# Kernel tuning notes

Hardware: AMD Instinct MI355X
Metric: run time of the kernel (lower is better)

Reference implementation:

```python
import jax, jax.numpy as jnp
import numpy as np

# config
B, V, S, D = 2, 8, 256, 2048
NH, NKV, KVR = 32, 8, 2
HD = D // NH            # 64
G = NH // NKV           # GQA group size = 4
INIT = 0.02


def _neighbor_idx():
    # replicates generate_neighbor: left neighbors (i-half..i-1) then right (i+1..i+half), circular
    half = KVR // 2
    offsets = np.concatenate([np.arange(-half, 0), np.arange(1, half + 1)])
    return (np.arange(V)[:, None] + offsets[None, :]) % V  # [V, KVR]


def setup_inputs() -> dict:
    key = jax.random.key(0)
    k1, k2, k3, k4 = jax.random.split(key, 4)
    x = jax.random.normal(k1, (B, V, S, D), jnp.float32)
    wq = jax.random.normal(k2, (D, NH * HD), jnp.float32) * INIT
    wkv = jax.random.normal(k3, (D, 2 * NKV * HD), jnp.float32) * INIT
    wo = jax.random.normal(k4, (D, D), jnp.float32) * INIT
    return {"x": x, "wq": wq, "wkv": wkv, "wo": wo}


def reference(x, wq, wkv, wo):
    b, v, s, d = x.shape
    idx = _neighbor_idx()  # [V, KVR] static

    # Q projection: [b, v, s, NH*HD]
    xq = (x @ wq).reshape(b, v, s, NKV, G, HD)  # grouped-query layout (kv head, group)

    # neighbor gather: [b, v, KVR, s, d] -> [b, v, KVR*s, d]
    x_kv = x[:, idx].reshape(b, v, KVR * s, d)
    kv = x_kv @ wkv
    xk, xv = jnp.split(kv, 2, axis=-1)
    xk = xk.reshape(b, v, KVR * s, NKV, HD)
    xv = xv.reshape(b, v, KVR * s, NKV, HD)

    # grouped-query SDPA (no mask, eval mode): avoids materializing repeated K/V
    scale = 1.0 / jnp.sqrt(jnp.asarray(HD, x.dtype))
    scores = jnp.einsum('bvsngh,bvtnh->bvngst', xq, xk) * scale  # [b,v,NKV,G,s,KVR*s]
    attn = jax.nn.softmax(scores, axis=-1)
    out = jnp.einsum('bvngst,bvtnh->bvsngh', attn, xv).reshape(b, v, s, d)
    return out @ wo
```

## Files before the change

### kernel.cpp

```cpp
#include <hip/hip_runtime.h>
#include <stdint.h>

typedef unsigned short u16;
typedef unsigned int   u32;
typedef short short8 __attribute__((ext_vector_type(8)));
typedef float f32x4  __attribute__((ext_vector_type(4)));

__device__ __forceinline__ u16 f2bf(float f){
  u32 u = __builtin_bit_cast(u32, f);
  u32 r = (u + 0x7FFFu + ((u >> 16) & 1u)) >> 16;
  return (u16)r;
}
__device__ __forceinline__ u32 cvtpk(float a, float b){
  u32 r; asm("v_cvt_pk_bf16_f32 %0, %1, %2" : "=v"(r) : "v"(a), "v"(b)); return r;
}
__device__ __forceinline__ void gload16(const u16* g, u16* l){
  __builtin_amdgcn_global_load_lds((const __attribute__((address_space(1))) void*)g,
                                   (__attribute__((address_space(3))) void*)l, 16, 0, 0);
}
#define BARRIER()  do{ __builtin_amdgcn_s_barrier(); __builtin_amdgcn_sched_barrier(0); }while(0)

__global__ __launch_bounds__(256) void k_cvt_bf16(const float* __restrict__ x,
                                                  u16* __restrict__ y, int n8){
  int i = blockIdx.x * 256 + threadIdx.x;
  if (i >= n8) return;
  const float4* p = (const float4*)x + (size_t)i * 2;
  float4 a = p[0], b = p[1];
  short8 o;
  o[0] = f2bf(a.x); o[1] = f2bf(a.y); o[2] = f2bf(a.z); o[3] = f2bf(a.w);
  o[4] = f2bf(b.x); o[5] = f2bf(b.y); o[6] = f2bf(b.z); o[7] = f2bf(b.w);
  *(short8*)(y + (size_t)i * 8) = o;
}

__global__ __launch_bounds__(256) void k_transpose_w(const float* __restrict__ in,
                                                     u16* __restrict__ out, int R, int C){
  __shared__ float tile[32][33];
  int nc = C >> 5;
  int cb = blockIdx.x % nc, rb = blockIdx.x / nc;
  int tx = threadIdx.x & 31, ty = threadIdx.x >> 5;
#pragma unroll
  for (int i = 0; i < 4; ++i){
    int r = rb * 32 + ty + i * 8;
    tile[ty + i * 8][tx] = in[(size_t)r * C + cb * 32 + tx];
  }
  __syncthreads();
#pragma unroll
  for (int i = 0; i < 4; ++i){
    int c = cb * 32 + ty + i * 8;
    out[(size_t)c * R + rb * 32 + tx] = f2bf(tile[tx][ty + i * 8]);
  }
}

template<int BM, int BN, int MH, int NFRAG, int ALOADS, int BLOADS, bool QSCALE, typename CT>
__global__ __launch_bounds__(512, 1) void k_gemm8p(const u16* __restrict__ A,
                                                   const u16* __restrict__ Bt,
                                                   CT* __restrict__ C,
                                                   int N, int K){
  constexpr int SZA = BM * 128;
  constexpr int SZB = BN * 128;
  constexpr int SZ  = SZA + SZB;
  constexpr int WTM = BM / 2;
  constexpr int WTN = BN / 4;
  __shared__ char lds[2 * SZ];

  int tid = threadIdx.x, lane = tid & 63, wid = tid >> 6;
  int l16 = lane & 15, g4 = lane >> 4;
  int wm = wid >> 2, wn = wid & 3;
  int bid = blockIdx.x;
  int wg = (bid & 7) * 32 + (bid >> 3);
  int nb = N / BN;
  int bm = wg / nb, bn = wg % nb;

  const u16* baseA = A  + (size_t)(bm * BM) * K;
  const u16* baseB = Bt + (size_t)(bn * BN) * K;

  int aLds[ALOADS], aG[ALOADS];
#pragma unroll
  for (int i = 0; i < ALOADS; ++i){
    int q = (wid * ALOADS + i) * 1024 + lane * 16;
    int row = q >> 7, c = q & 127;
    int cs = c ^ ((row & 7) << 4);
    aLds[i] = q; aG[i] = row * K + (cs >> 1);
  }
  int bLds[BLOADS], bG[BLOADS];
#pragma unroll
  for (int j = 0; j < BLOADS; ++j){
    int q = (wid * BLOADS + j) * 1024 + lane * 16;
    int row = q >> 7, c = q & 127;
    int cs = c ^ ((row & 7) << 4);
    bLds[j] = q; bG[j] = row * K + (cs >> 1);
  }
  auto stageA = [&](int t){
    char* dst = lds + (t & 1) * SZ;
#pragma unroll
    for (int i = 0; i < ALOADS; ++i) gload16(baseA + aG[i] + t * 64, (u16*)(dst + aLds[i]));
  };
  auto stageB = [&](int t){
    char* dst = lds + (t & 1) * SZ + SZA;
#pragma unroll
    for (int j = 0; j < BLOADS; ++j) gload16(baseB + bG[j] + t * 64, (u16*)(dst + bLds[j]));
  };
  auto rdA = [&](const char* Ab, int m, int ks){
    int row = wm * WTM + m * 16 + l16;
    return *(const short8*)(Ab + row * 128 + ((ks * 64 + g4 * 16) ^ ((row & 7) << 4)));
  };
  auto rdB = [&](const char* Bb, int nf, int ks){
    int row = wn * WTN + nf * 16 + l16;
    return *(const short8*)(Bb + row * 128 + ((ks * 64 + g4 * 16) ^ ((row & 7) << 4)));
  };

  f32x4 zero4 = {0.f, 0.f, 0.f, 0.f};
  f32x4 acc[2 * MH][NFRAG];
#pragma unroll
  for (int i = 0; i < 2 * MH; ++i)
#pragma unroll
    for (int j = 0; j < NFRAG; ++j) acc[i][j] = zero4;

  int NK = K >> 6;
  stageA(0); stageB(0);
  asm volatile("s_waitcnt vmcnt(0)" ::: "memory");
  BARRIER();
  short8 a0[MH], a1[MH], a2[MH], a3[MH], bf0[NFRAG], bf1[NFRAG];
#pragma unroll
  for (int nf = 0; nf < NFRAG; ++nf) bf0[nf] = rdB(lds + SZA, nf, 0);
#pragma unroll
  for (int m = 0; m < MH; ++m)       a0[m]  = rdA(lds, m, 0);

  for (int kt = 0; kt < NK; ++kt){
    const char* Ab = lds + (kt & 1) * SZ;
    const char* Bb = Ab + SZA;
    bool st = (kt + 1 < NK);
#pragma unroll
    for (int m = 0; m < MH; ++m) a1[m] = rdA(Ab, MH + m, 0);
    if (st) stageA(kt + 1);
    BARRIER();
    __builtin_amdgcn_s_setprio(1);
#pragma unroll
    for (int m = 0; m < MH; ++m)
#pragma unroll
      for (int nf = 0; nf < NFRAG; ++nf)
        acc[m][nf] = __builtin_amdgcn_mfma_f32_16x16x32_bf16(a0[m], bf0[nf], acc[m][nf], 0, 0, 0);
    __builtin_amdgcn_s_setprio(0);
#pragma unroll
    for (int nf = 0; nf < NFRAG; ++nf) bf1[nf] = rdB(Bb, nf, 1);
#pragma unroll
    for (int m = 0; m < MH; ++m)       a2[m]  = rdA(Ab, m, 1);
    if (st) stageB(kt + 1);
    BARRIER();
    __builtin_amdgcn_s_setprio(1);
#pragma unroll
    for (int m = 0; m < MH; ++m)
#pragma unroll
      for (int nf = 0; nf < NFRAG; ++nf)
        acc[MH + m][nf] = __builtin_amdgcn_mfma_f32_16x16x32_bf16(a1[m], bf0[nf], acc[MH + m][nf], 0, 0, 0);
    __builtin_amdgcn_s_setprio(0);
#pragma unroll
    for (int m = 0; m < MH; ++m) a3[m] = rdA(Ab, MH + m, 1);
    BARRIER();
    __builtin_amdgcn_s_setprio(1);
#pragma unroll
    for (int m = 0; m < MH; ++m)
#pragma unroll
      for (int nf = 0; nf < NFRAG; ++nf)
        acc[m][nf] = __builtin_amdgcn_mfma_f32_16x16x32_bf16(a2[m], bf1[nf], acc[m][nf], 0, 0, 0);
    __builtin_amdgcn_s_setprio(0);
    if (st) asm volatile("s_waitcnt vmcnt(0)" ::: "memory");
    BARRIER();
    if (st){
      const char* Ab2 = lds + ((kt + 1) & 1) * SZ;
      const char* Bb2 = Ab2 + SZA;
#pragma unroll
      for (int nf = 0; nf < NFRAG; ++nf) bf0[nf] = rdB(Bb2, nf, 0);
#pragma unroll
      for (int m = 0; m < MH; ++m)       a0[m]  = rdA(Ab2, m, 0);
    }
    __builtin_amdgcn_s_setprio(1);
#pragma unroll
    for (int m = 0; m < MH; ++m)
#pragma unroll
      for (int nf = 0; nf < NFRAG; ++nf)
        acc[MH + m][nf] = __builtin_amdgcn_mfma_f32_16x16x32_bf16(a3[m], bf1[nf], acc[MH + m][nf], 0, 0, 0);
    __builtin_amdgcn_s_setprio(0);
    BARRIER();
  }

#pragma unroll
  for (int mf = 0; mf < 2 * MH; ++mf)
#pragma unroll
    for (int nf = 0; nf < NFRAG; ++nf)
#pragma unroll
      for (int r = 0; r < 4; ++r){
        int row = bm * BM + wm * WTM + mf * 16 + g4 * 4 + r;
        int col = bn * BN + wn * WTN + nf * 16 + l16;
        float vv = acc[mf][nf][r];
        if constexpr (QSCALE) { if (col < 2048) vv *= 0.18033688011112042f; }
        if constexpr (sizeof(CT) == 2) C[(size_t)row * N + col] = (CT)f2bf(vv);
        else                           C[(size_t)row * N + col] = (CT)vv;
      }
}

__global__ __launch_bounds__(256) void k_vt(const u16* __restrict__ c1, u16* __restrict__ vt){
  __shared__ u16 tile[64][72];
  int bid = blockIdx.x;
  int st = bid & 3, n = (bid >> 2) & 7, bv = bid >> 5;
  int t = threadIdx.x;
  int sr = t >> 2, sc = t & 3;
  const u16* src = c1 + (size_t)(bv * 256 + st * 64 + sr) * 3072 + 2560 + n * 64 + sc * 16;
  short8 a = *(const short8*)src;
  short8 b = *(const short8*)(src + 8);
  *(short8*)&tile[sr][sc * 16]     = a;
  *(short8*)&tile[sr][sc * 16 + 8] = b;
  __syncthreads();
  int h = t >> 2, c2 = t & 3;
  short8 o0, o1;
#pragma unroll
  for (int j = 0; j < 8; ++j) o0[j] = (short)tile[c2 * 16 + j][h];
#pragma unroll
  for (int j = 0; j < 8; ++j) o1[j] = (short)tile[c2 * 16 + 8 + j][h];
  u16* dst = vt + (size_t)((bv * 8 + n) * 64 + h) * 256 + st * 64 + c2 * 16;
  *(short8*)dst       = o0;
  *(short8*)(dst + 8) = o1;
}

__global__ __launch_bounds__(256, 2) void k_attn(const u16* __restrict__ c1,
                                                 const u16* __restrict__ vt,
                                                 u16* __restrict__ att){
  __shared__ u16 Klds[64][72];
  __shared__ u16 Vlds[64][72];
  __shared__ u16 Plds[4][16][72];
  int bid = blockIdx.x;
  int qt = bid & 3, n = (bid >> 2) & 7, v = (bid >> 5) & 7, b = bid >> 8;
  int tid = threadIdx.x;
  int g = tid >> 6, lane = tid & 63, l16 = lane & 15, g4 = lane >> 4;
  int bv = b * 8 + v;
  int rowQ = bv * 256 + qt * 64;
  int qcol = n * 256 + g * 64;

  short8 qf[4][2];
#pragma unroll
  for (int qi = 0; qi < 4; ++qi)
#pragma unroll
    for (int kk = 0; kk < 2; ++kk)
      qf[qi][kk] = *(const short8*)(c1 + (size_t)(rowQ + qi * 16 + l16) * 3072
                                     + qcol + kk * 32 + g4 * 8);

  f32x4 zero4 = {0.f, 0.f, 0.f, 0.f};
  f32x4 O[4][4];
#pragma unroll
  for (int i = 0; i < 4; ++i)
#pragma unroll
    for (int j = 0; j < 4; ++j) O[i][j] = zero4;
  float m2[4]   = {-3.0e38f, -3.0e38f, -3.0e38f, -3.0e38f};
  float lsum[4] = {0.f, 0.f, 0.f, 0.f};

  int sr = tid >> 2, sc = tid & 3;
  short8 k0, k1, v0, v1;
  {
    int vn = (v + 7) & 7;
    const u16* ks = c1 + (size_t)((b * 8 + vn) * 256 + sr) * 3072 + 2048 + n * 64 + sc * 16;
    k0 = *(const short8*)ks; k1 = *(const short8*)(ks + 8);
    const u16* vs = vt + (size_t)(((b * 8 + vn) * 8 + n) * 64 + sr) * 256 + sc * 16;
    v0 = *(const short8*)vs; v1 = *(const short8*)(vs + 8);
  }

  for (int ti = 0; ti < 8; ++ti){
    __syncthreads();
    *(short8*)&Klds[sr][sc * 16]     = k0;
    *(short8*)&Klds[sr][sc * 16 + 8] = k1;
    *(short8*)&Vlds[sr][sc * 16]     = v0;
    *(short8*)&Vlds[sr][sc * 16 + 8] = v1;
    __syncthreads();
    if (ti < 7){
      int tn = ti + 1;
      int vn = (tn < 4) ? ((v + 7) & 7) : ((v + 1) & 7);
      int tb = (tn & 3) * 64;
      const u16* ks = c1 + (size_t)((b * 8 + vn) * 256 + tb + sr) * 3072 + 2048 + n * 64 + sc * 16;
      k0 = *(const short8*)ks; k1 = *(const short8*)(ks + 8);
      const u16* vs = vt + (size_t)(((b * 8 + vn) * 8 + n) * 64 + sr) * 256 + tb + sc * 16;
      v0 = *(const short8*)vs; v1 = *(const short8*)(vs + 8);
    }
    short8 kf[4][2], vf[2][4];
#pragma unroll
    for (int kt = 0; kt < 4; ++kt)
#pragma unroll
      for (int ks = 0; ks < 2; ++ks)
        kf[kt][ks] = *(const short8*)&Klds[kt * 16 + l16][ks * 32 + g4 * 8];
#pragma unroll
    for (int ks = 0; ks < 2; ++ks)
#pragma unroll
      for (int hi = 0; hi < 4; ++hi)
        vf[ks][hi] = *(const short8*)&Vlds[hi * 16 + l16][ks * 32 + g4 * 8];

#pragma unroll
    for (int qi = 0; qi < 4; ++qi){
      f32x4 sa[4];
#pragma unroll
      for (int kt = 0; kt < 4; ++kt){
        sa[kt] = zero4;
#pragma unroll
        for (int ks = 0; ks < 2; ++ks)
          sa[kt] = __builtin_amdgcn_mfma_f32_16x16x32_bf16(kf[kt][ks], qf[qi][ks], sa[kt], 0, 0, 0);
      }
      float pmax = sa[0][0];
#pragma unroll
      for (int kt = 0; kt < 4; ++kt)
#pragma unroll
        for (int r = 0; r < 4; ++r) pmax = fmaxf(pmax, sa[kt][r]);
      pmax = fmaxf(pmax, __shfl_xor(pmax, 16));
      pmax = fmaxf(pmax, __shfl_xor(pmax, 32));
      if (__any(pmax > m2[qi] + 8.f)){
        float mnew  = fmaxf(m2[qi], pmax);
        float alpha = exp2f(m2[qi] - mnew);
        m2[qi] = mnew;
        lsum[qi] *= alpha;
        float ab[4];
#pragma unroll
        for (int r = 0; r < 4; ++r) ab[r] = __shfl(alpha, g4 * 4 + r);
#pragma unroll
        for (int hi = 0; hi < 4; ++hi)
#pragma unroll
          for (int r = 0; r < 4; ++r) O[qi][hi][r] *= ab[r];
      }
      float m = m2[qi];
      float psum = 0.f;
      u32 w[4][2];
#pragma unroll
      for (int kt = 0; kt < 4; ++kt){
        float p0 = exp2f(sa[kt][0] - m);
        float p1 = exp2f(sa[kt][1] - m);
        float p2 = exp2f(sa[kt][2] - m);
        float p3 = exp2f(sa[kt][3] - m);
        psum += (p0 + p1) + (p2 + p3);
        w[kt][0] = cvtpk(p0, p1);
        w[kt][1] = cvtpk(p2, p3);
      }
      psum += __shfl_xor(psum, 16);
      psum += __shfl_xor(psum, 32);
      lsum[qi] += psum;
      u32* prow = (u32*)&Plds[g][l16][0];
#pragma unroll
      for (int kt = 0; kt < 4; ++kt){
        prow[kt * 8 + g4 * 2]     = w[kt][0];
        prow[kt * 8 + g4 * 2 + 1] = w[kt][1];
      }
      short8 pa[2];
#pragma unroll
      for (int ks = 0; ks < 2; ++ks)
        pa[ks] = *(const short8*)&Plds[g][l16][ks * 32 + g4 * 8];
#pragma unroll
      for (int hi = 0; hi < 4; ++hi)
#pragma unroll
        for (int ks = 0; ks < 2; ++ks)
          O[qi][hi] = __builtin_amdgcn_mfma_f32_16x16x32_bf16(pa[ks], vf[ks][hi], O[qi][hi], 0, 0, 0);
    }
  }
#pragma unroll
  for (int qi = 0; qi < 4; ++qi){
    float lb[4];
#pragma unroll
    for (int r = 0; r < 4; ++r) lb[r] = 1.0f / __shfl(lsum[qi], g4 * 4 + r);
#pragma unroll
    for (int hi = 0; hi < 4; ++hi)
#pragma unroll
      for (int r = 0; r < 4; ++r){
        int row = rowQ + qi * 16 + g4 * 4 + r;
        int col = qcol + hi * 16 + l16;
        att[(size_t)row * 2048 + col] = f2bf(O[qi][hi][r] * lb[r]);
      }
  }
}

extern "C" void kernel_launch(void* const* d_in, const int* in_sizes, int n_in,
                              void* d_out, int out_size, void* d_ws, size_t ws_size,
                              hipStream_t stream){
  const float* x   = (const float*)d_in[0];
  const float* wq  = (const float*)d_in[1];
  const float* wkv = (const float*)d_in[2];
  const float* wo  = (const float*)d_in[3];
  float* out = (float*)d_out;
  char* ws = (char*)d_ws;

  u16* x_bf  = (u16*)(ws);
  u16* wqkvt = (u16*)(ws + 16777216);
  u16* wot   = (u16*)(ws + 29360128);
  u16* c1    = (u16*)(ws + 37748736);
  u16* vt    = (u16*)(ws + 62914560);
  u16* att   = x_bf;

  k_cvt_bf16<<<4096, 256, 0, stream>>>(x, x_bf, 1048576);
  k_transpose_w<<<4096, 256, 0, stream>>>(wq,  wqkvt,               2048, 2048);
  k_transpose_w<<<2048, 256, 0, stream>>>(wkv, wqkvt + 2048 * 2048, 2048, 1024);
  k_transpose_w<<<4096, 256, 0, stream>>>(wo,  wot,                 2048, 2048);
  k_gemm8p<256, 192, 4, 3, 4, 3, true,  u16  ><<<256, 512, 0, stream>>>(x_bf, wqkvt, c1, 3072, 2048);
  k_vt<<<512, 256, 0, stream>>>(c1, vt);
  k_attn<<<512, 256, 0, stream>>>(c1, vt, att);
  k_gemm8p<128, 256, 2, 4, 2, 4, false, float><<<256, 512, 0, stream>>>(att, wot, out, 2048, 2048);
}
```

Before: 154.7 us.

## Pre-swizzle weights into MFMA fragment order and load B directly to registers

The weight-transpose kernels become a prep kernel that writes bf16 weights in the exact per-wave MFMA fragment layout. The GEMM then loads B fragments straight from global memory into registers, prefetched one k-tile ahead, instead of staging them through LDS. This removes B LDS traffic and its share of the LDS footprint, so more waves may fit per CU now that the launch bound no longer forces one block. The cost is more register pressure for the double-buffered B fragments, and B reuse across the two wave rows now depends on the cache instead of LDS.

```diff
diff --git a/kernel.cpp b/kernel.cpp
--- a/kernel.cpp
+++ b/kernel.cpp
@@ -32,36 +32,45 @@
   *(short8*)(y + (size_t)i * 8) = o;
 }
 
-__global__ __launch_bounds__(256) void k_transpose_w(const float* __restrict__ in,
-                                                     u16* __restrict__ out, int R, int C){
-  __shared__ float tile[32][33];
+template<int MODE>
+__global__ __launch_bounds__(256) void k_prepw(const float* __restrict__ w,
+                                               u16* __restrict__ Bp, int C, int noff){
+  __shared__ float tile[64][33];
   int nc = C >> 5;
-  int cb = blockIdx.x % nc, rb = blockIdx.x / nc;
-  int tx = threadIdx.x & 31, ty = threadIdx.x >> 5;
-#pragma unroll
-  for (int i = 0; i < 4; ++i){
-    int r = rb * 32 + ty + i * 8;
-    tile[ty + i * 8][tx] = in[(size_t)r * C + cb * 32 + tx];
-  }
+  int cb = blockIdx.x % nc;
+  int kt = blockIdx.x / nc;
+  int t = threadIdx.x;
+  int kl = t >> 5, c = t & 31;
+#pragma unroll
+  for (int i = 0; i < 8; ++i)
+    tile[kl + i * 8][c] = w[(size_t)(kt * 64 + kl + i * 8) * C + cb * 32 + c];
   __syncthreads();
-#pragma unroll
-  for (int i = 0; i < 4; ++i){
-    int c = cb * 32 + ty + i * 8;
-    out[(size_t)c * R + rb * 32 + tx] = f2bf(tile[tx][ty + i * 8]);
-  }
-}
-
-template<int BM, int BN, int MH, int NFRAG, int ALOADS, int BLOADS, bool QSCALE, typename CT>
-__global__ __launch_bounds__(512, 1) void k_gemm8p(const u16* __restrict__ A,
-                                                   const u16* __restrict__ Bt,
-                                                   CT* __restrict__ C,
-                                                   int N, int K){
+  int l16 = t & 15, g4 = (t >> 4) & 3, ks = (t >> 6) & 1, nh = t >> 7;
+  int n = noff + cb * 32 + nh * 16 + l16;
+  int kb = ks * 32 + g4 * 8;
+  short8 o;
+#pragma unroll
+  for (int e = 0; e < 8; ++e) o[e] = (short)f2bf(tile[kb + e][nh * 16 + l16]);
+  size_t dst;
+  if constexpr (MODE == 0){
+    int bn = n / 192, r = n % 192, wn = r / 48, r2 = r % 48, nf = r2 / 16, L = r2 % 16;
+    dst = ((((size_t)(bn * 4 + wn) * 32 + kt) * 2 + ks) * 3 + nf) * 512 + (g4 * 16 + L) * 8;
+  } else {
+    int bn = n >> 8, wn = (n >> 6) & 3, nf = (n >> 4) & 3, L = n & 15;
+    dst = ((((size_t)(bn * 4 + wn) * 32 + kt) * 2 + ks) * 4 + nf) * 512 + (g4 * 16 + L) * 8;
+  }
+  *(short8*)(Bp + dst) = o;
+}
+
+template<int BM, int NF, int MH, int ALOADS, bool QSCALE, typename CT>
+__global__ __launch_bounds__(512) void k_gemm_bd(const u16* __restrict__ A,
+                                                 const u16* __restrict__ Bp,
+                                                 CT* __restrict__ C,
+                                                 int N, int K){
+  constexpr int BN  = NF * 64;
+  constexpr int WTM = BM / 2;
   constexpr int SZA = BM * 128;
-  constexpr int SZB = BN * 128;
-  constexpr int SZ  = SZA + SZB;
-  constexpr int WTM = BM / 2;
-  constexpr int WTN = BN / 4;
-  __shared__ char lds[2 * SZ];
+  __shared__ char lds[2 * SZA];
 
   int tid = threadIdx.x, lane = tid & 63, wid = tid >> 6;
   int l16 = lane & 15, g4 = lane >> 4;
@@ -71,8 +80,8 @@
   int nb = N / BN;
   int bm = wg / nb, bn = wg % nb;
 
-  const u16* baseA = A  + (size_t)(bm * BM) * K;
-  const u16* baseB = Bt + (size_t)(bn * BN) * K;
+  const u16* baseA  = A  + (size_t)(bm * BM) * K;
+  const u16* baseBp = Bp + (size_t)(bn * 4 + wn) * (32 * 2 * NF * 512) + lane * 8;
 
   int aLds[ALOADS], aG[ALOADS];
 #pragma unroll
@@ -82,116 +91,106 @@
     int cs = c ^ ((row & 7) << 4);
     aLds[i] = q; aG[i] = row * K + (cs >> 1);
   }
-  int bLds[BLOADS], bG[BLOADS];
-#pragma unroll
-  for (int j = 0; j < BLOADS; ++j){
-    int q = (wid * BLOADS + j) * 1024 + lane * 16;
-    int row = q >> 7, c = q & 127;
-    int cs = c ^ ((row & 7) << 4);
-    bLds[j] = q; bG[j] = row * K + (cs >> 1);
-  }
   auto stageA = [&](int t){
-    char* dst = lds + (t & 1) * SZ;
+    char* dst = lds + (t & 1) * SZA;
 #pragma unroll
     for (int i = 0; i < ALOADS; ++i) gload16(baseA + aG[i] + t * 64, (u16*)(dst + aLds[i]));
-  };
-  auto stageB = [&](int t){
-    char* dst = lds + (t & 1) * SZ + SZA;
-#pragma unroll
-    for (int j = 0; j < BLOADS; ++j) gload16(baseB + bG[j] + t * 64, (u16*)(dst + bLds[j]));
   };
   auto rdA = [&](const char* Ab, int m, int ks){
     int row = wm * WTM + m * 16 + l16;
     return *(const short8*)(Ab + row * 128 + ((ks * 64 + g4 * 16) ^ ((row & 7) << 4)));
   };
-  auto rdB = [&](const char* Bb, int nf, int ks){
-    int row = wn * WTN + nf * 16 + l16;
-    return *(const short8*)(Bb + row * 128 + ((ks * 64 + g4 * 16) ^ ((row & 7) << 4)));
+  auto loadB = [&](short8* dst, int t){
+    const u16* p = baseBp + (size_t)t * (2 * NF * 512);
+#pragma unroll
+    for (int j = 0; j < 2 * NF; ++j) dst[j] = *(const short8*)(p + j * 512);
   };
 
   f32x4 zero4 = {0.f, 0.f, 0.f, 0.f};
-  f32x4 acc[2 * MH][NFRAG];
+  f32x4 acc[2 * MH][NF];
 #pragma unroll
   for (int i = 0; i < 2 * MH; ++i)
 #pragma unroll
-    for (int j = 0; j < NFRAG; ++j) acc[i][j] = zero4;
+    for (int j = 0; j < NF; ++j) acc[i][j] = zero4;
+
+  short8 bf[2 * NF], bfn[2 * NF];
+  short8 ac[MH], an[MH], a2[MH], a3[MH];
 
   int NK = K >> 6;
-  stageA(0); stageB(0);
+  stageA(0);
+  loadB(bf, 0);
   asm volatile("s_waitcnt vmcnt(0)" ::: "memory");
   BARRIER();
-  short8 a0[MH], a1[MH], a2[MH], a3[MH], bf0[NFRAG], bf1[NFRAG];
-#pragma unroll
-  for (int nf = 0; nf < NFRAG; ++nf) bf0[nf] = rdB(lds + SZA, nf, 0);
-#pragma unroll
-  for (int m = 0; m < MH; ++m)       a0[m]  = rdA(lds, m, 0);
+#pragma unroll
+  for (int m = 0; m < MH; ++m) ac[m] = rdA(lds, m, 0);
 
   for (int kt = 0; kt < NK; ++kt){
-    const char* Ab = lds + (kt & 1) * SZ;
-    const char* Bb = Ab + SZA;
+    const char* Ab = lds + (kt & 1) * SZA;
     bool st = (kt + 1 < NK);
 #pragma unroll
-    for (int m = 0; m < MH; ++m) a1[m] = rdA(Ab, MH + m, 0);
+    for (int m = 0; m < MH; ++m) an[m] = rdA(Ab, MH + m, 0);
     if (st) stageA(kt + 1);
     BARRIER();
     __builtin_amdgcn_s_setprio(1);
 #pragma unroll
     for (int m = 0; m < MH; ++m)
 #pragma unroll
-      for (int nf = 0; nf < NFRAG; ++nf)
-        acc[m][nf] = __builtin_amdgcn_mfma_f32_16x16x32_bf16(a0[m], bf0[nf], acc[m][nf], 0, 0, 0);
+      for (int nf = 0; nf < NF; ++nf)
+        acc[m][nf] = __builtin_amdgcn_mfma_f32_16x16x32_bf16(ac[m], bf[nf], acc[m][nf], 0, 0, 0);
     __builtin_amdgcn_s_setprio(0);
 #pragma unroll
-    for (int nf = 0; nf < NFRAG; ++nf) bf1[nf] = rdB(Bb, nf, 1);
-#pragma unroll
-    for (int m = 0; m < MH; ++m)       a2[m]  = rdA(Ab, m, 1);
-    if (st) stageB(kt + 1);
+    for (int m = 0; m < MH; ++m) a2[m] = rdA(Ab, m, 1);
     BARRIER();
     __builtin_amdgcn_s_setprio(1);
 #pragma unroll
     for (int m = 0; m < MH; ++m)
 #pragma unroll
-      for (int nf = 0; nf < NFRAG; ++nf)
-        acc[MH + m][nf] = __builtin_amdgcn_mfma_f32_16x16x32_bf16(a1[m], bf0[nf], acc[MH + m][nf], 0, 0, 0);
+      for (int nf = 0; nf < NF; ++nf)
+        acc[MH + m][nf] = __builtin_amdgcn_mfma_f32_16x16x32_bf16(an[m], bf[nf], acc[MH + m][nf], 0, 0, 0);
     __builtin_amdgcn_s_setprio(0);
 #pragma unroll
     for (int m = 0; m < MH; ++m) a3[m] = rdA(Ab, MH + m, 1);
+    if (st) loadB(bfn, kt + 1);
     BARRIER();
     __builtin_amdgcn_s_setprio(1);
 #pragma unroll
     for (int m = 0; m < MH; ++m)
 #pragma unroll
-      for (int nf = 0; nf < NFRAG; ++nf)
-        acc[m][nf] = __builtin_amdgcn_mfma_f32_16x16x32_bf16(a2[m], bf1[nf], acc[m][nf], 0, 0, 0);
+      for (int nf = 0; nf < NF; ++nf)
+        acc[m][nf] = __builtin_amdgcn_mfma_f32_16x16x32_bf16(a2[m], bf[NF + nf], acc[m][nf], 0, 0, 0);
     __builtin_amdgcn_s_setprio(0);
-    if (st) asm volatile("s_waitcnt vmcnt(0)" ::: "memory");
-    BARRIER();
     if (st){
-      const char* Ab2 = lds + ((kt + 1) & 1) * SZ;
-      const char* Bb2 = Ab2 + SZA;
-#pragma unroll
-      for (int nf = 0; nf < NFRAG; ++nf) bf0[nf] = rdB(Bb2, nf, 0);
-#pragma unroll
-      for (int m = 0; m < MH; ++m)       a0[m]  = rdA(Ab2, m, 0);
+      if constexpr (NF == 3) asm volatile("s_waitcnt vmcnt(6)" ::: "memory");
+      else                   asm volatile("s_waitcnt vmcnt(8)" ::: "memory");
+    }
+    BARRIER();
+    if (st){
+      const char* Ab2 = lds + ((kt + 1) & 1) * SZA;
+#pragma unroll
+      for (int m = 0; m < MH; ++m) ac[m] = rdA(Ab2, m, 0);
     }
     __builtin_amdgcn_s_setprio(1);
 #pragma unroll
     for (int m = 0; m < MH; ++m)
 #pragma unroll
-      for (int nf = 0; nf < NFRAG; ++nf)
-        acc[MH + m][nf] = __builtin_amdgcn_mfma_f32_16x16x32_bf16(a3[m], bf1[nf], acc[MH + m][nf], 0, 0, 0);
+      for (int nf = 0; nf < NF; ++nf)
+        acc[MH + m][nf] = __builtin_amdgcn_mfma_f32_16x16x32_bf16(a3[m], bf[NF + nf], acc[MH + m][nf], 0, 0, 0);
     __builtin_amdgcn_s_setprio(0);
+    if (st){
+#pragma unroll
+      for (int j = 0; j < 2 * NF; ++j) bf[j] = bfn[j];
+    }
     BARRIER();
   }
 
 #pragma unroll
   for (int mf = 0; mf < 2 * MH; ++mf)
 #pragma unroll
-    for (int nf = 0; nf < NFRAG; ++nf)
+    for (int nf = 0; nf < NF; ++nf)
 #pragma unroll
       for (int r = 0; r < 4; ++r){
         int row = bm * BM + wm * WTM + mf * 16 + g4 * 4 + r;
-        int col = bn * BN + wn * WTN + nf * 16 + l16;
+        int col = bn * BN + wn * (NF * 16) + nf * 16 + l16;
         float vv = acc[mf][nf][r];
         if constexpr (QSCALE) { if (col < 2048) vv *= 0.18033688011112042f; }
         if constexpr (sizeof(CT) == 2) C[(size_t)row * N + col] = (CT)f2bf(vv);
@@ -380,19 +379,19 @@
   float* out = (float*)d_out;
   char* ws = (char*)d_ws;
 
-  u16* x_bf  = (u16*)(ws);
-  u16* wqkvt = (u16*)(ws + 16777216);
-  u16* wot   = (u16*)(ws + 29360128);
-  u16* c1    = (u16*)(ws + 37748736);
-  u16* vt    = (u16*)(ws + 62914560);
-  u16* att   = x_bf;
+  u16* x_bf   = (u16*)(ws);
+  u16* bp_qkv = (u16*)(ws + 16777216);
+  u16* bp_o   = (u16*)(ws + 29360128);
+  u16* c1     = (u16*)(ws + 37748736);
+  u16* vt     = (u16*)(ws + 62914560);
+  u16* att    = x_bf;
 
   k_cvt_bf16<<<4096, 256, 0, stream>>>(x, x_bf, 1048576);
-  k_transpose_w<<<4096, 256, 0, stream>>>(wq,  wqkvt,               2048, 2048);
-  k_transpose_w<<<2048, 256, 0, stream>>>(wkv, wqkvt + 2048 * 2048, 2048, 1024);
-  k_transpose_w<<<4096, 256, 0, stream>>>(wo,  wot,                 2048, 2048);
-  k_gemm8p<256, 192, 4, 3, 4, 3, true,  u16  ><<<256, 512, 0, stream>>>(x_bf, wqkvt, c1, 3072, 2048);
+  k_prepw<0><<<2048, 256, 0, stream>>>(wq,  bp_qkv, 2048, 0);
+  k_prepw<0><<<1024, 256, 0, stream>>>(wkv, bp_qkv, 1024, 2048);
+  k_prepw<1><<<2048, 256, 0, stream>>>(wo,  bp_o,   2048, 0);
+  k_gemm_bd<256, 3, 4, 4, true,  u16  ><<<256, 512, 0, stream>>>(x_bf, bp_qkv, c1, 3072, 2048);
   k_vt<<<512, 256, 0, stream>>>(c1, vt);
   k_attn<<<512, 256, 0, stream>>>(c1, vt, att);
-  k_gemm8p<128, 256, 2, 4, 2, 4, false, float><<<256, 512, 0, stream>>>(att, wot, out, 2048, 2048);
-}
+  k_gemm_bd<128, 4, 2, 2, false, float><<<256, 512, 0, stream>>>(att, bp_o, out, 2048, 2048);
+}
```

New measurement: 180.7 us. 16.8% more time.

## Restructure GEMM main loop with finer-grained staged loads and partial vmcnt waits

Applied to the files above, without the earlier changes.

Replaces the GEMM kernel with a variant that splits next-tile global-to-LDS loads into per-slab stages spread across the four MFMA phases. It uses partial s_waitcnt vmcnt counts instead of a full drain before the buffer swap. It also changes the A-tile row-to-wave mapping and the LDS load addressing, and drops the min-blocks launch bound. The aim is to overlap global loads with MFMA work more evenly and reduce stalls at barriers. This adds extra barriers per k-step and risks correctness if the partial wait counts do not cover the slabs that are read next.

```diff
diff --git a/kernel.cpp b/kernel.cpp
--- a/kernel.cpp
+++ b/kernel.cpp
@@ -51,16 +51,16 @@
   }
 }
 
-template<int BM, int BN, int MH, int NFRAG, int ALOADS, int BLOADS, bool QSCALE, typename CT>
-__global__ __launch_bounds__(512, 1) void k_gemm8p(const u16* __restrict__ A,
-                                                   const u16* __restrict__ Bt,
-                                                   CT* __restrict__ C,
-                                                   int N, int K){
+template<int BM, int BN, int MFR, int NF, bool QSCALE, typename CT>
+__global__ __launch_bounds__(512) void k_gemm8m(const u16* __restrict__ A,
+                                                const u16* __restrict__ Bt,
+                                                CT* __restrict__ C,
+                                                int N, int K){
+  constexpr int MH  = MFR / 2;
+  constexpr int AL  = BM / 64, BL = BN / 64, L = AL + BL;
   constexpr int SZA = BM * 128;
-  constexpr int SZB = BN * 128;
-  constexpr int SZ  = SZA + SZB;
-  constexpr int WTM = BM / 2;
-  constexpr int WTN = BN / 4;
+  constexpr int SZ  = (BM + BN) * 128;
+  constexpr int F3  = (MFR == 8) ? 2 : 1;
   __shared__ char lds[2 * SZ];
 
   int tid = threadIdx.x, lane = tid & 63, wid = tid >> 6;
@@ -74,124 +74,133 @@
   const u16* baseA = A  + (size_t)(bm * BM) * K;
   const u16* baseB = Bt + (size_t)(bn * BN) * K;
 
-  int aLds[ALOADS], aG[ALOADS];
-#pragma unroll
-  for (int i = 0; i < ALOADS; ++i){
-    int q = (wid * ALOADS + i) * 1024 + lane * 16;
+  int aG[AL], bG[BL];
+#pragma unroll
+  for (int i = 0; i < AL; ++i){
+    int q = i * 8192 + tid * 16;
     int row = q >> 7, c = q & 127;
     int cs = c ^ ((row & 7) << 4);
-    aLds[i] = q; aG[i] = row * K + (cs >> 1);
-  }
-  int bLds[BLOADS], bG[BLOADS];
-#pragma unroll
-  for (int j = 0; j < BLOADS; ++j){
-    int q = (wid * BLOADS + j) * 1024 + lane * 16;
+    aG[i] = row * K + (cs >> 1);
+  }
+#pragma unroll
+  for (int j = 0; j < BL; ++j){
+    int q = j * 8192 + tid * 16;
     int row = q >> 7, c = q & 127;
     int cs = c ^ ((row & 7) << 4);
-    bLds[j] = q; bG[j] = row * K + (cs >> 1);
-  }
-  auto stageA = [&](int t){
+    bG[j] = row * K + (cs >> 1);
+  }
+  auto stageL = [&](int t, int l){
     char* dst = lds + (t & 1) * SZ;
-#pragma unroll
-    for (int i = 0; i < ALOADS; ++i) gload16(baseA + aG[i] + t * 64, (u16*)(dst + aLds[i]));
+    if (l < BL){
+      gload16(baseB + bG[l] + t * 64, (u16*)(dst + SZA + l * 8192 + tid * 16));
+    } else {
+      int i;
+      if constexpr (MFR == 8){ constexpr int ord[4] = {0, 2, 1, 3}; i = ord[l - BL]; }
+      else                   { i = l - BL; }
+      gload16(baseA + aG[i] + t * 64, (u16*)(dst + i * 8192 + tid * 16));
+    }
   };
-  auto stageB = [&](int t){
-    char* dst = lds + (t & 1) * SZ + SZA;
-#pragma unroll
-    for (int j = 0; j < BLOADS; ++j) gload16(baseB + bG[j] + t * 64, (u16*)(dst + bLds[j]));
+  auto aRowBase = [&](int mf){
+    if constexpr (MFR == 8) return wm * 128 + mf * 16;
+    else                    return (mf >> 1) * 64 + wm * 32 + (mf & 1) * 16;
   };
-  auto rdA = [&](const char* Ab, int m, int ks){
-    int row = wm * WTM + m * 16 + l16;
-    return *(const short8*)(Ab + row * 128 + ((ks * 64 + g4 * 16) ^ ((row & 7) << 4)));
+  auto rdA = [&](const char* buf, int mf, int ks){
+    int row = aRowBase(mf) + l16;
+    return *(const short8*)(buf + row * 128 + ((ks * 64 + g4 * 16) ^ ((row & 7) << 4)));
   };
-  auto rdB = [&](const char* Bb, int nf, int ks){
-    int row = wn * WTN + nf * 16 + l16;
-    return *(const short8*)(Bb + row * 128 + ((ks * 64 + g4 * 16) ^ ((row & 7) << 4)));
+  auto rdB = [&](const char* buf, int nf, int ks){
+    int row = wn * (NF * 16) + nf * 16 + l16;
+    return *(const short8*)(buf + SZA + row * 128 + ((ks * 64 + g4 * 16) ^ ((row & 7) << 4)));
   };
 
   f32x4 zero4 = {0.f, 0.f, 0.f, 0.f};
-  f32x4 acc[2 * MH][NFRAG];
-#pragma unroll
-  for (int i = 0; i < 2 * MH; ++i)
-#pragma unroll
-    for (int j = 0; j < NFRAG; ++j) acc[i][j] = zero4;
+  f32x4 acc[MFR][NF];
+#pragma unroll
+  for (int i = 0; i < MFR; ++i)
+#pragma unroll
+    for (int j = 0; j < NF; ++j) acc[i][j] = zero4;
 
   int NK = K >> 6;
-  stageA(0); stageB(0);
+#pragma unroll
+  for (int l = 0; l < L; ++l) stageL(0, l);
   asm volatile("s_waitcnt vmcnt(0)" ::: "memory");
   BARRIER();
-  short8 a0[MH], a1[MH], a2[MH], a3[MH], bf0[NFRAG], bf1[NFRAG];
-#pragma unroll
-  for (int nf = 0; nf < NFRAG; ++nf) bf0[nf] = rdB(lds + SZA, nf, 0);
-#pragma unroll
-  for (int m = 0; m < MH; ++m)       a0[m]  = rdA(lds, m, 0);
-
+
+  short8 av[MH], bv[NF];
   for (int kt = 0; kt < NK; ++kt){
-    const char* Ab = lds + (kt & 1) * SZ;
-    const char* Bb = Ab + SZA;
+    const char* buf = lds + (kt & 1) * SZ;
     bool st = (kt + 1 < NK);
 #pragma unroll
-    for (int m = 0; m < MH; ++m) a1[m] = rdA(Ab, MH + m, 0);
-    if (st) stageA(kt + 1);
+    for (int nf = 0; nf < NF; ++nf) bv[nf] = rdB(buf, nf, 0);
+#pragma unroll
+    for (int m = 0; m < MH; ++m)    av[m] = rdA(buf, m, 0);
+    if (st){ stageL(kt + 1, 0); stageL(kt + 1, 1); }
     BARRIER();
     __builtin_amdgcn_s_setprio(1);
 #pragma unroll
     for (int m = 0; m < MH; ++m)
 #pragma unroll
-      for (int nf = 0; nf < NFRAG; ++nf)
-        acc[m][nf] = __builtin_amdgcn_mfma_f32_16x16x32_bf16(a0[m], bf0[nf], acc[m][nf], 0, 0, 0);
+      for (int nf = 0; nf < NF; ++nf)
+        acc[m][nf] = __builtin_amdgcn_mfma_f32_16x16x32_bf16(av[m], bv[nf], acc[m][nf], 0, 0, 0);
     __builtin_amdgcn_s_setprio(0);
-#pragma unroll
-    for (int nf = 0; nf < NFRAG; ++nf) bf1[nf] = rdB(Bb, nf, 1);
-#pragma unroll
-    for (int m = 0; m < MH; ++m)       a2[m]  = rdA(Ab, m, 1);
-    if (st) stageB(kt + 1);
+    if (st) asm volatile("s_waitcnt vmcnt(2)" ::: "memory");
+    else    asm volatile("s_waitcnt vmcnt(0)" ::: "memory");
+    BARRIER();
+#pragma unroll
+    for (int m = 0; m < MH; ++m) av[m] = rdA(buf, MH + m, 0);
+    if (st){ stageL(kt + 1, 2); stageL(kt + 1, 3); }
     BARRIER();
     __builtin_amdgcn_s_setprio(1);
 #pragma unroll
     for (int m = 0; m < MH; ++m)
 #pragma unroll
-      for (int nf = 0; nf < NFRAG; ++nf)
-        acc[MH + m][nf] = __builtin_amdgcn_mfma_f32_16x16x32_bf16(a1[m], bf0[nf], acc[MH + m][nf], 0, 0, 0);
+      for (int nf = 0; nf < NF; ++nf)
+        acc[MH + m][nf] = __builtin_amdgcn_mfma_f32_16x16x32_bf16(av[m], bv[nf], acc[MH + m][nf], 0, 0, 0);
     __builtin_amdgcn_s_setprio(0);
-#pragma unroll
-    for (int m = 0; m < MH; ++m) a3[m] = rdA(Ab, MH + m, 1);
+    BARRIER();
+#pragma unroll
+    for (int nf = 0; nf < NF; ++nf) bv[nf] = rdB(buf, nf, 1);
+#pragma unroll
+    for (int m = 0; m < MH; ++m)    av[m] = rdA(buf, m, 1);
+    if (st){
+#pragma unroll
+      for (int l = 4; l < L - 1; ++l) stageL(kt + 1, l);
+    }
     BARRIER();
     __builtin_amdgcn_s_setprio(1);
 #pragma unroll
     for (int m = 0; m < MH; ++m)
 #pragma unroll
-      for (int nf = 0; nf < NFRAG; ++nf)
-        acc[m][nf] = __builtin_amdgcn_mfma_f32_16x16x32_bf16(a2[m], bf1[nf], acc[m][nf], 0, 0, 0);
+      for (int nf = 0; nf < NF; ++nf)
+        acc[m][nf] = __builtin_amdgcn_mfma_f32_16x16x32_bf16(av[m], bv[nf], acc[m][nf], 0, 0, 0);
     __builtin_amdgcn_s_setprio(0);
-    if (st) asm volatile("s_waitcnt vmcnt(0)" ::: "memory");
-    BARRIER();
+    BARRIER();
+#pragma unroll
+    for (int m = 0; m < MH; ++m) av[m] = rdA(buf, MH + m, 1);
+    if (st) stageL(kt + 1, L - 1);
+    BARRIER();
+    __builtin_amdgcn_s_setprio(1);
+#pragma unroll
+    for (int m = 0; m < MH; ++m)
+#pragma unroll
+      for (int nf = 0; nf < NF; ++nf)
+        acc[MH + m][nf] = __builtin_amdgcn_mfma_f32_16x16x32_bf16(av[m], bv[nf], acc[MH + m][nf], 0, 0, 0);
+    __builtin_amdgcn_s_setprio(0);
     if (st){
-      const char* Ab2 = lds + ((kt + 1) & 1) * SZ;
-      const char* Bb2 = Ab2 + SZA;
-#pragma unroll
-      for (int nf = 0; nf < NFRAG; ++nf) bf0[nf] = rdB(Bb2, nf, 0);
-#pragma unroll
-      for (int m = 0; m < MH; ++m)       a0[m]  = rdA(Ab2, m, 0);
+      if constexpr (F3 == 2) asm volatile("s_waitcnt vmcnt(2)" ::: "memory");
+      else                   asm volatile("s_waitcnt vmcnt(1)" ::: "memory");
     }
-    __builtin_amdgcn_s_setprio(1);
-#pragma unroll
-    for (int m = 0; m < MH; ++m)
-#pragma unroll
-      for (int nf = 0; nf < NFRAG; ++nf)
-        acc[MH + m][nf] = __builtin_amdgcn_mfma_f32_16x16x32_bf16(a3[m], bf1[nf], acc[MH + m][nf], 0, 0, 0);
-    __builtin_amdgcn_s_setprio(0);
-    BARRIER();
-  }
-
-#pragma unroll
-  for (int mf = 0; mf < 2 * MH; ++mf)
-#pragma unroll
-    for (int nf = 0; nf < NFRAG; ++nf)
+    BARRIER();
+  }
+
+#pragma unroll
+  for (int mf = 0; mf < MFR; ++mf)
+#pragma unroll
+    for (int nf = 0; nf < NF; ++nf)
 #pragma unroll
       for (int r = 0; r < 4; ++r){
-        int row = bm * BM + wm * WTM + mf * 16 + g4 * 4 + r;
-        int col = bn * BN + wn * WTN + nf * 16 + l16;
+        int row = bm * BM + aRowBase(mf) + g4 * 4 + r;
+        int col = bn * BN + wn * (NF * 16) + nf * 16 + l16;
         float vv = acc[mf][nf][r];
         if constexpr (QSCALE) { if (col < 2048) vv *= 0.18033688011112042f; }
         if constexpr (sizeof(CT) == 2) C[(size_t)row * N + col] = (CT)f2bf(vv);
@@ -391,8 +400,8 @@
   k_transpose_w<<<4096, 256, 0, stream>>>(wq,  wqkvt,               2048, 2048);
   k_transpose_w<<<2048, 256, 0, stream>>>(wkv, wqkvt + 2048 * 2048, 2048, 1024);
   k_transpose_w<<<4096, 256, 0, stream>>>(wo,  wot,                 2048, 2048);
-  k_gemm8p<256, 192, 4, 3, 4, 3, true,  u16  ><<<256, 512, 0, stream>>>(x_bf, wqkvt, c1, 3072, 2048);
+  k_gemm8m<256, 192, 8, 3, true,  u16  ><<<256, 512, 0, stream>>>(x_bf, wqkvt, c1, 3072, 2048);
   k_vt<<<512, 256, 0, stream>>>(c1, vt);
   k_attn<<<512, 256, 0, stream>>>(c1, vt, att);
-  k_gemm8p<128, 256, 2, 4, 2, 4, false, float><<<256, 512, 0, stream>>>(att, wot, out, 2048, 2048);
-}
+  k_gemm8m<128, 256, 4, 4, false, float><<<256, 512, 0, stream>>>(att, wot, out, 2048, 2048);
+}
```

After: 155.5 us. Within noise of the previous version (+0.5%).
